# Performance work log

Measured on AMD Instinct MI355X. Metric: run time of the kernel, lower is better.

## Reference

```python
import jax, jax.numpy as jnp
import numpy as np

B, L, D, DK, T = 8192, 64, 512, 64, 128
WIDE_IN = 2 * T + T * T  # 16640


def setup_inputs() -> dict:
    key = jax.random.key(0)
    ks = jax.random.split(key, 24)
    s = 0.02
    inp = {
        "mashup_tags": jax.random.uniform(ks[0], (B, T), jnp.float32),
        "target_api_tags": jax.random.uniform(ks[1], (B, T), jnp.float32),
        "cross_product_tag": jax.random.uniform(ks[2], (B, T * T), jnp.float32),
        "encoded_api_context": jax.random.normal(ks[3], (B, L, D), jnp.float32),
        "candidate_api_description_feature": jax.random.normal(ks[4], (B, D), jnp.float32),
        "mashup_description_feature": jax.random.normal(ks[5], (B, D), jnp.float32),
        "context_len": jax.random.randint(ks[6], (B,), 0, L + 1, jnp.int64 if jax.config.jax_enable_x64 else jnp.int32),
        # attention projections (torch Linear weight layout: [out, in], no bias)
        "W_K": s * jax.random.normal(ks[7], (DK, D), jnp.float32),
        "W_Q": s * jax.random.normal(ks[8], (DK, D), jnp.float32),
        # wide head
        "wide_w": s * jax.random.normal(ks[9], (1, WIDE_IN), jnp.float32),
        "wide_b": jnp.zeros((1,), jnp.float32),
        # deep MLP 1536->512->256->128->1
        "d1_w": s * jax.random.normal(ks[10], (512, 3 * D), jnp.float32),
        "d1_b": jnp.zeros((512,), jnp.float32),
        "d2_w": s * jax.random.normal(ks[11], (256, 512), jnp.float32),
        "d2_b": jnp.zeros((256,), jnp.float32),
        "d3_w": s * jax.random.normal(ks[12], (128, 256), jnp.float32),
        "d3_b": jnp.zeros((128,), jnp.float32),
        "d4_w": s * jax.random.normal(ks[13], (1, 128), jnp.float32),
        "d4_b": jnp.zeros((1,), jnp.float32),
        "wide_weight": jnp.ones((1,), jnp.float32),
        "deep_weight": jnp.ones((1,), jnp.float32),
        "bias": jnp.zeros((1,), jnp.float32),
    }
    return inp


def reference(mashup_tags, target_api_tags, cross_product_tag,
              encoded_api_context, candidate_api_description_feature,
              mashup_description_feature, context_len,
              W_K, W_Q, wide_w, wide_b,
              d1_w, d1_b, d2_w, d2_b, d3_w, d3_b, d4_w, d4_b,
              wide_weight, deep_weight, bias):
    # ---- wide branch ----
    wide_in = jnp.concatenate([mashup_tags, target_api_tags, cross_product_tag], axis=1)
    wide_out = jax.nn.sigmoid(wide_in @ wide_w.T + wide_b)  # (B,1)

    # ---- ragged attention (vectorized masked softmax replaces the Python batch loop) ----
    K = jnp.einsum("bld,kd->blk", encoded_api_context, W_K)          # (B,L,dk)
    Q = candidate_api_description_feature @ W_Q.T                     # (B,dk)
    scores = jnp.einsum("blk,bk->bl", K, Q)                           # (B,L)
    mask = jnp.arange(scores.shape[1])[None, :] < context_len[:, None]
    m = jnp.max(jnp.where(mask, scores, -1e30), axis=-1, keepdims=True)
    e = jnp.where(mask, jnp.exp(scores - m), 0.0)
    denom = jnp.sum(e, axis=-1, keepdims=True)
    probs = e / jnp.maximum(denom, 1e-30)  # rows with length==0 -> all zeros (matches torch zeros fallback)
    api_context = jnp.einsum("bl,bld->bd", probs, encoded_api_context)  # (B,512)

    # ---- deep branch ----
    deep_in = jnp.concatenate([mashup_description_feature, api_context,
                               candidate_api_description_feature], axis=1)  # (B,1536)
    h = jax.nn.relu(deep_in @ d1_w.T + d1_b)
    h = jax.nn.relu(h @ d2_w.T + d2_b)
    h = jax.nn.relu(h @ d3_w.T + d3_b)
    deep_out = h @ d4_w.T + d4_b  # (B,1)

    out = wide_weight * wide_out + deep_weight * deep_out + bias
    return jax.nn.sigmoid(out)
```

## Files before the change

kernel.cpp:

```cpp
#include <hip/hip_runtime.h>

#define Bsz 8192
#define Lctx 64
#define Ddim 512
#define DK 64
#define Ttag 128
#define RQT 2

using f32x4 = __attribute__((ext_vector_type(4))) float;
using bf16x8 = __attribute__((ext_vector_type(8))) short;

__device__ __forceinline__ float wave_sum(float v) {
#pragma unroll
    for (int m = 32; m > 0; m >>= 1) v += __shfl_xor(v, m, 64);
    return v;
}

__device__ __forceinline__ float dot4(float4 a, float4 b) {
    return a.x * b.x + a.y * b.y + a.z * b.z + a.w * b.w;
}

__device__ __forceinline__ unsigned f2bf(float f) {
    unsigned int u = __float_as_uint(f);
    u = u + 0x7fffu + ((u >> 16) & 1u);
    return u >> 16;
}
__device__ __forceinline__ unsigned pack2(float a, float b) {
    return f2bf(a) | (f2bf(b) << 16);
}
__device__ __forceinline__ float bflo(unsigned int v) { return __uint_as_float(v << 16); }
__device__ __forceinline__ float bfhi(unsigned int v) { return __uint_as_float(v & 0xffff0000u); }
__device__ __forceinline__ float bf2f(unsigned short u) { return __uint_as_float((unsigned)u << 16); }

__global__ __launch_bounds__(256) void k_f2bf(
    const float* __restrict__ s, unsigned short* __restrict__ d, int n4)
{
    const int i = blockIdx.x * 256 + threadIdx.x;
    if (i < n4) {
        const float4 v = ((const float4*)s)[i];
        uint2 w;
        w.x = pack2(v.x, v.y);
        w.y = pack2(v.z, v.w);
        *(uint2*)&d[(size_t)i * 4] = w;
    }
}

__global__ __launch_bounds__(256) void k_qtilde(
    const float* __restrict__ C, const float* __restrict__ WQ,
    const float* __restrict__ WK, float* __restrict__ qt)
{
    const int lane = threadIdx.x & 63;
    const int gw = blockIdx.x * 4 + (threadIdx.x >> 6);
    const int b0 = gw * RQT;

    float4 c0[RQT], c1[RQT];
#pragma unroll
    for (int r = 0; r < RQT; ++r) {
        const float4* row = (const float4*)(C + (size_t)(b0 + r) * Ddim);
        c0[r] = row[lane];
        c1[r] = row[64 + lane];
    }
    float tv[RQT];
#pragma unroll
    for (int r = 0; r < RQT; ++r) tv[r] = 0.f;
    for (int k = 0; k < DK; ++k) {
        const float4* wrow = (const float4*)(WQ + (size_t)k * Ddim);
        const float4 w0 = wrow[lane];
        const float4 w1 = wrow[64 + lane];
#pragma unroll
        for (int r = 0; r < RQT; ++r) {
            float p = dot4(c0[r], w0) + dot4(c1[r], w1);
            p = wave_sum(p);
            if (lane == k) tv[r] = p;
        }
    }
    float4 a0[RQT], a1[RQT];
#pragma unroll
    for (int r = 0; r < RQT; ++r) {
        a0[r] = make_float4(0.f, 0.f, 0.f, 0.f);
        a1[r] = make_float4(0.f, 0.f, 0.f, 0.f);
    }
    for (int k = 0; k < DK; ++k) {
        const float4* wrow = (const float4*)(WK + (size_t)k * Ddim);
        const float4 w0 = wrow[lane];
        const float4 w1 = wrow[64 + lane];
#pragma unroll
        for (int r = 0; r < RQT; ++r) {
            const float tk = __shfl(tv[r], k, 64);
            a0[r].x += tk * w0.x; a0[r].y += tk * w0.y;
            a0[r].z += tk * w0.z; a0[r].w += tk * w0.w;
            a1[r].x += tk * w1.x; a1[r].y += tk * w1.y;
            a1[r].z += tk * w1.z; a1[r].w += tk * w1.w;
        }
    }
#pragma unroll
    for (int r = 0; r < RQT; ++r) {
        float4* orow = (float4*)(qt + (size_t)(b0 + r) * Ddim);
        orow[lane] = a0[r];
        orow[64 + lane] = a1[r];
    }
}

__global__ __launch_bounds__(256, 2) void k_attn(
    const float* __restrict__ X, const float* __restrict__ qt,
    const int* __restrict__ clen, const float* __restrict__ mdesc,
    const float* __restrict__ cand, unsigned short* __restrict__ din)
{
    __shared__ float sl[Lctx];
    __shared__ float pl[Lctx];
    __shared__ float part[4][Ddim];

    const int b = blockIdx.x;
    const int tid = threadIdx.x;
    const int wave = tid >> 6, lane = tid & 63;

    const float4* qrow = (const float4*)(qt + (size_t)b * Ddim);
    const float4 q0 = qrow[lane];
    const float4 q1 = qrow[64 + lane];
    const float4* xb = (const float4*)(X + (size_t)b * Lctx * Ddim);

    uint2 pk[16][2];
    float sc[16];

#pragma unroll
    for (int g = 0; g < 4; ++g) {
        float4 t0[4], t1[4];
#pragma unroll
        for (int i = 0; i < 4; ++i) {
            const int l = wave * 16 + g * 4 + i;
            t0[i] = xb[l * 128 + lane];
            t1[i] = xb[l * 128 + 64 + lane];
        }
#pragma unroll
        for (int i = 0; i < 4; ++i) {
            const int r = g * 4 + i;
            sc[r] = dot4(t0[i], q0) + dot4(t1[i], q1);
            pk[r][0].x = pack2(t0[i].x, t0[i].y);
            pk[r][0].y = pack2(t0[i].z, t0[i].w);
            pk[r][1].x = pack2(t1[i].x, t1[i].y);
            pk[r][1].y = pack2(t1[i].z, t1[i].w);
        }
    }
#pragma unroll
    for (int r = 0; r < 16; ++r) sc[r] = wave_sum(sc[r]);
    if (lane == 0) {
#pragma unroll
        for (int r = 0; r < 16; ++r) sl[wave * 16 + r] = sc[r];
    }
    __syncthreads();

    const int len = clen[b];
    float m = -1e30f;
    for (int l = 0; l < len; ++l) m = fmaxf(m, sl[l]);
    float denom = 0.f;
    for (int l = 0; l < len; ++l) denom += __expf(sl[l] - m);
    const float rden = 1.f / fmaxf(denom, 1e-30f);
    if (tid < Lctx) pl[tid] = (tid < len) ? __expf(sl[tid] - m) * rden : 0.f;
    __syncthreads();

    float4 a0 = make_float4(0.f, 0.f, 0.f, 0.f);
    float4 a1 = make_float4(0.f, 0.f, 0.f, 0.f);
#pragma unroll
    for (int r = 0; r < 16; ++r) {
        const float p = pl[wave * 16 + r];
        a0.x += p * bflo(pk[r][0].x); a0.y += p * bfhi(pk[r][0].x);
        a0.z += p * bflo(pk[r][0].y); a0.w += p * bfhi(pk[r][0].y);
        a1.x += p * bflo(pk[r][1].x); a1.y += p * bfhi(pk[r][1].x);
        a1.z += p * bflo(pk[r][1].y); a1.w += p * bfhi(pk[r][1].y);
    }
    *(float4*)&part[wave][lane * 4] = a0;
    *(float4*)&part[wave][256 + lane * 4] = a1;
    __syncthreads();

    unsigned short* dr = din + (size_t)b * 1536;
    {
        const int d0 = tid * 2;
        const float2 s0 = *(const float2*)&part[0][d0];
        const float2 s1 = *(const float2*)&part[1][d0];
        const float2 s2 = *(const float2*)&part[2][d0];
        const float2 s3 = *(const float2*)&part[3][d0];
        const float vx = s0.x + s1.x + s2.x + s3.x;
        const float vy = s0.y + s1.y + s2.y + s3.y;
        *(unsigned*)&dr[512 + d0] = pack2(vx, vy);
    }
    {
        const float4 v = (tid < 128)
            ? ((const float4*)(mdesc + (size_t)b * Ddim))[tid]
            : ((const float4*)(cand + (size_t)b * Ddim))[tid - 128];
        uint2 w;
        w.x = pack2(v.x, v.y);
        w.y = pack2(v.z, v.w);
        const int off = (tid < 128) ? tid * 4 : 1024 + (tid - 128) * 4;
        *(uint2*)&dr[off] = w;
    }
}

__global__ __launch_bounds__(256) void k_wide(
    const float* __restrict__ mt, const float* __restrict__ tt,
    const float* __restrict__ cp, const float* __restrict__ ww,
    const float* __restrict__ wb, float* __restrict__ wl)
{
    const int b = blockIdx.x;
    const int tid = threadIdx.x;
    const int wave = tid >> 6, lane = tid & 63;
    float acc = 0.f;
    if (tid < 64) {
        float4 v;
        if (tid < 32) v = ((const float4*)(mt + (size_t)b * Ttag))[tid];
        else          v = ((const float4*)(tt + (size_t)b * Ttag))[tid - 32];
        const float4 w = ((const float4*)ww)[tid];
        acc += dot4(v, w);
    }
    const float4* cp4 = (const float4*)(cp + (size_t)b * (Ttag * Ttag));
    const float4* ww4 = (const float4*)(ww + 2 * Ttag);
#pragma unroll 4
    for (int i = tid; i < (Ttag * Ttag) / 4; i += 256)
        acc += dot4(cp4[i], ww4[i]);
    acc = wave_sum(acc);
    __shared__ float red[4];
    if (lane == 0) red[wave] = acc;
    __syncthreads();
    if (tid == 0) wl[b] = red[0] + red[1] + red[2] + red[3] + wb[0];
}

__global__ __launch_bounds__(256) void k_gemm_bf16(
    const unsigned short* __restrict__ A, const unsigned short* __restrict__ W,
    const float* __restrict__ bias, unsigned short* __restrict__ C,
    const int K, const int N, const int relu)
{
    __shared__ unsigned short As[128][72];
    __shared__ unsigned short Bs[128][72];
    const int tid = threadIdx.x;
    const int wave = tid >> 6, lane = tid & 63;
    const int wm = wave >> 1, wn = wave & 1;
    const size_t m0 = (size_t)blockIdx.x * 128;
    const size_t n0 = (size_t)blockIdx.y * 128;

    f32x4 acc[4][4];
#pragma unroll
    for (int i = 0; i < 4; ++i)
#pragma unroll
        for (int j = 0; j < 4; ++j) acc[i][j] = (f32x4){0.f, 0.f, 0.f, 0.f};

    uint4 pa[4], pb[4];
    auto loadA = [&](int k0) {
#pragma unroll
        for (int j = 0; j < 4; ++j) {
            const int i = tid + j * 256;
            const int row = i >> 3, c8 = (i & 7) * 8;
            pa[j] = *(const uint4*)(A + (m0 + row) * (size_t)K + k0 + c8);
        }
    };
    auto loadB = [&](int k0) {
#pragma unroll
        for (int j = 0; j < 4; ++j) {
            const int i = tid + j * 256;
            const int row = i >> 3, c8 = (i & 7) * 8;
            pb[j] = *(const uint4*)(W + (n0 + row) * (size_t)K + k0 + c8);
        }
    };

    loadA(0);
    loadB(0);
    for (int k0 = 0; k0 < K; k0 += 64) {
        __syncthreads();
#pragma unroll
        for (int j = 0; j < 4; ++j) {
            const int i = tid + j * 256;
            const int row = i >> 3, c8 = (i & 7) * 8;
            *(uint4*)&As[row][c8] = pa[j];
            *(uint4*)&Bs[row][c8] = pb[j];
        }
        __syncthreads();
        if (k0 + 64 < K) { loadA(k0 + 64); loadB(k0 + 64); }
#pragma unroll
        for (int kk = 0; kk < 2; ++kk) {
            const int krow = kk * 32 + (lane >> 4) * 8;
            bf16x8 af[4], bfr[4];
#pragma unroll
            for (int mm = 0; mm < 4; ++mm)
                af[mm] = *(const bf16x8*)&As[wm * 64 + mm * 16 + (lane & 15)][krow];
#pragma unroll
            for (int nn = 0; nn < 4; ++nn)
                bfr[nn] = *(const bf16x8*)&Bs[wn * 64 + nn * 16 + (lane & 15)][krow];
#pragma unroll
            for (int mm = 0; mm < 4; ++mm)
#pragma unroll
                for (int nn = 0; nn < 4; ++nn)
                    acc[mm][nn] = __builtin_amdgcn_mfma_f32_16x16x32_bf16(
                        af[mm], bfr[nn], acc[mm][nn], 0, 0, 0);
        }
    }

#pragma unroll
    for (int nn = 0; nn < 4; ++nn) {
        const int col = (int)n0 + wn * 64 + nn * 16 + (lane & 15);
        const float bv = bias[col];
#pragma unroll
        for (int mm = 0; mm < 4; ++mm) {
#pragma unroll
            for (int r = 0; r < 4; ++r) {
                const size_t row = m0 + wm * 64 + mm * 16 + (lane >> 4) * 4 + r;
                float v = acc[mm][nn][r] + bv;
                if (relu) v = fmaxf(v, 0.f);
                C[row * N + col] = (unsigned short)f2bf(v);
            }
        }
    }
}

__global__ __launch_bounds__(256) void k_final(
    const unsigned short* __restrict__ h3, const float* __restrict__ d4w,
    const float* __restrict__ d4b, const float* __restrict__ wl,
    const float* __restrict__ wwt, const float* __restrict__ dwt,
    const float* __restrict__ bs, float* __restrict__ out)
{
    const int lane = threadIdx.x & 63;
    const int b = blockIdx.x * 4 + (threadIdx.x >> 6);
    const unsigned short* hr = h3 + (size_t)b * 128;
    float v = bf2f(hr[lane]) * d4w[lane] + bf2f(hr[64 + lane]) * d4w[64 + lane];
    v = wave_sum(v);
    if (lane == 0) {
        const float deep = v + d4b[0];
        const float wo = 1.f / (1.f + __expf(-wl[b]));
        const float z = wwt[0] * wo + dwt[0] * deep + bs[0];
        out[b] = 1.f / (1.f + __expf(-z));
    }
}

extern "C" void kernel_launch(void* const* d_in, const int* in_sizes, int n_in,
                              void* d_out, int out_size, void* d_ws, size_t ws_size,
                              hipStream_t stream)
{
    const float* mt    = (const float*)d_in[0];
    const float* tt    = (const float*)d_in[1];
    const float* cp    = (const float*)d_in[2];
    const float* X     = (const float*)d_in[3];
    const float* cand  = (const float*)d_in[4];
    const float* mdesc = (const float*)d_in[5];
    const int*   clen  = (const int*)d_in[6];
    const float* WK    = (const float*)d_in[7];
    const float* WQ    = (const float*)d_in[8];
    const float* ww    = (const float*)d_in[9];
    const float* wb    = (const float*)d_in[10];
    const float* d1w   = (const float*)d_in[11];
    const float* d1b   = (const float*)d_in[12];
    const float* d2w   = (const float*)d_in[13];
    const float* d2b   = (const float*)d_in[14];
    const float* d3w   = (const float*)d_in[15];
    const float* d3b   = (const float*)d_in[16];
    const float* d4w   = (const float*)d_in[17];
    const float* d4b   = (const float*)d_in[18];
    const float* wwt   = (const float*)d_in[19];
    const float* dwt   = (const float*)d_in[20];
    const float* bs    = (const float*)d_in[21];
    float* out = (float*)d_out;

    char* w = (char*)d_ws;
    unsigned short* din = (unsigned short*)w;            w += (size_t)Bsz * 1536 * 2;
    float* qt           = (float*)w;                     w += (size_t)Bsz * 512 * 4;
    unsigned short* h1  = (unsigned short*)w;            w += (size_t)Bsz * 512 * 2;
    unsigned short* h2  = (unsigned short*)w;            w += (size_t)Bsz * 256 * 2;
    unsigned short* h3  = (unsigned short*)w;            w += (size_t)Bsz * 128 * 2;
    float* wl           = (float*)w;                     w += (size_t)Bsz * 4;
    unsigned short* w1b = (unsigned short*)w;            w += (size_t)512 * 1536 * 2;
    unsigned short* w2b = (unsigned short*)w;            w += (size_t)256 * 512 * 2;
    unsigned short* w3b = (unsigned short*)w;            w += (size_t)128 * 256 * 2;

    hipLaunchKernelGGL(k_f2bf, dim3(768), dim3(256), 0, stream, d1w, w1b, 512 * 1536 / 4);
    hipLaunchKernelGGL(k_f2bf, dim3(128), dim3(256), 0, stream, d2w, w2b, 256 * 512 / 4);
    hipLaunchKernelGGL(k_f2bf, dim3(32),  dim3(256), 0, stream, d3w, w3b, 128 * 256 / 4);

    hipLaunchKernelGGL(k_qtilde, dim3(Bsz / (RQT * 4)), dim3(256), 0, stream,
                       cand, WQ, WK, qt);
    hipLaunchKernelGGL(k_attn, dim3(Bsz), dim3(256), 0, stream,
                       X, qt, clen, mdesc, cand, din);
    hipLaunchKernelGGL(k_wide, dim3(Bsz), dim3(256), 0, stream,
                       mt, tt, cp, ww, wb, wl);
    hipLaunchKernelGGL(k_gemm_bf16, dim3(64, 4), dim3(256), 0, stream,
                       din, w1b, d1b, h1, 1536, 512, 1);
    hipLaunchKernelGGL(k_gemm_bf16, dim3(64, 2), dim3(256), 0, stream,
                       h1, w2b, d2b, h2, 512, 256, 1);
    hipLaunchKernelGGL(k_gemm_bf16, dim3(64, 1), dim3(256), 0, stream,
                       h2, w3b, d3b, h3, 256, 128, 1);
    hipLaunchKernelGGL(k_final, dim3(Bsz / 4), dim3(256), 0, stream,
                       h3, d4w, d4b, wl, wwt, dwt, bs, out);
}
```

Before: 473.9 us.

## Skip masked context rows, fuse wide head into attention, merge weight casts

The attention kernel now loads, scores and accumulates only context rows below context_len, so masked rows of the large encoded context tensor are never read from memory. The wide-branch dot product over the cross-product tags is folded into the same per-row kernel, removing one launch and overlapping its loads with the attention work. The three weight-cast kernels are merged into one launch. The risks are extra register pressure in the fused kernel and divergent predicated loads.

```diff
diff --git a/kernel.cpp b/kernel.cpp
--- a/kernel.cpp
+++ b/kernel.cpp
@@ -32,17 +32,23 @@
 __device__ __forceinline__ float bfhi(unsigned int v) { return __uint_as_float(v & 0xffff0000u); }
 __device__ __forceinline__ float bf2f(unsigned short u) { return __uint_as_float((unsigned)u << 16); }
 
-__global__ __launch_bounds__(256) void k_f2bf(
-    const float* __restrict__ s, unsigned short* __restrict__ d, int n4)
-{
-    const int i = blockIdx.x * 256 + threadIdx.x;
-    if (i < n4) {
-        const float4 v = ((const float4*)s)[i];
-        uint2 w;
-        w.x = pack2(v.x, v.y);
-        w.y = pack2(v.z, v.w);
-        *(uint2*)&d[(size_t)i * 4] = w;
-    }
+__global__ __launch_bounds__(256) void k_f2bf3(
+    const float* __restrict__ s1, unsigned short* __restrict__ d1,
+    const float* __restrict__ s2, unsigned short* __restrict__ d2,
+    const float* __restrict__ s3, unsigned short* __restrict__ d3)
+{
+    int i = blockIdx.x * 256 + threadIdx.x;
+    const float* s;
+    unsigned short* d;
+    if (i < 196608)      { s = s1; d = d1; }
+    else if (i < 229376) { i -= 196608; s = s2; d = d2; }
+    else if (i < 237568) { i -= 229376; s = s3; d = d3; }
+    else return;
+    const float4 v = ((const float4*)s)[i];
+    uint2 w;
+    w.x = pack2(v.x, v.y);
+    w.y = pack2(v.z, v.w);
+    *(uint2*)&d[(size_t)i * 4] = w;
 }
 
 __global__ __launch_bounds__(256) void k_qtilde(
@@ -101,18 +107,25 @@
     }
 }
 
-__global__ __launch_bounds__(256, 2) void k_attn(
+__global__ __launch_bounds__(256, 2) void k_attn_wide(
     const float* __restrict__ X, const float* __restrict__ qt,
     const int* __restrict__ clen, const float* __restrict__ mdesc,
-    const float* __restrict__ cand, unsigned short* __restrict__ din)
+    const float* __restrict__ cand,
+    const float* __restrict__ mt, const float* __restrict__ tt,
+    const float* __restrict__ cp, const float* __restrict__ ww,
+    const float* __restrict__ wb,
+    unsigned short* __restrict__ din, float* __restrict__ wl)
 {
     __shared__ float sl[Lctx];
     __shared__ float pl[Lctx];
     __shared__ float part[4][Ddim];
+    __shared__ float red[4];
 
     const int b = blockIdx.x;
     const int tid = threadIdx.x;
     const int wave = tid >> 6, lane = tid & 63;
+    const int len = clen[b];
+    const int nrows = min(16, max(0, len - wave * 16));
 
     const float4* qrow = (const float4*)(qt + (size_t)b * Ddim);
     const float4 q0 = qrow[lane];
@@ -124,32 +137,57 @@
 
 #pragma unroll
     for (int g = 0; g < 4; ++g) {
-        float4 t0[4], t1[4];
-#pragma unroll
-        for (int i = 0; i < 4; ++i) {
-            const int l = wave * 16 + g * 4 + i;
-            t0[i] = xb[l * 128 + lane];
-            t1[i] = xb[l * 128 + 64 + lane];
-        }
-#pragma unroll
-        for (int i = 0; i < 4; ++i) {
-            const int r = g * 4 + i;
-            sc[r] = dot4(t0[i], q0) + dot4(t1[i], q1);
-            pk[r][0].x = pack2(t0[i].x, t0[i].y);
-            pk[r][0].y = pack2(t0[i].z, t0[i].w);
-            pk[r][1].x = pack2(t1[i].x, t1[i].y);
-            pk[r][1].y = pack2(t1[i].z, t1[i].w);
-        }
-    }
-#pragma unroll
-    for (int r = 0; r < 16; ++r) sc[r] = wave_sum(sc[r]);
+        if (g * 4 < nrows) {
+            float4 t0[4], t1[4];
+#pragma unroll
+            for (int i = 0; i < 4; ++i) {
+                if (g * 4 + i < nrows) {
+                    const int l = wave * 16 + g * 4 + i;
+                    t0[i] = xb[l * 128 + lane];
+                    t1[i] = xb[l * 128 + 64 + lane];
+                }
+            }
+#pragma unroll
+            for (int i = 0; i < 4; ++i) {
+                if (g * 4 + i < nrows) {
+                    const int r = g * 4 + i;
+                    sc[r] = dot4(t0[i], q0) + dot4(t1[i], q1);
+                    pk[r][0].x = pack2(t0[i].x, t0[i].y);
+                    pk[r][0].y = pack2(t0[i].z, t0[i].w);
+                    pk[r][1].x = pack2(t1[i].x, t1[i].y);
+                    pk[r][1].y = pack2(t1[i].z, t1[i].w);
+                }
+            }
+        }
+    }
+#pragma unroll
+    for (int r = 0; r < 16; ++r)
+        if (r < nrows) sc[r] = wave_sum(sc[r]);
     if (lane == 0) {
 #pragma unroll
-        for (int r = 0; r < 16; ++r) sl[wave * 16 + r] = sc[r];
-    }
+        for (int r = 0; r < 16; ++r)
+            if (r < nrows) sl[wave * 16 + r] = sc[r];
+    }
+
+    float wacc = 0.f;
+    if (tid < 64) {
+        float4 v;
+        if (tid < 32) v = ((const float4*)(mt + (size_t)b * Ttag))[tid];
+        else          v = ((const float4*)(tt + (size_t)b * Ttag))[tid - 32];
+        wacc += dot4(v, ((const float4*)ww)[tid]);
+    }
+    {
+        const float4* cp4 = (const float4*)(cp + (size_t)b * (Ttag * Ttag));
+        const float4* ww4 = (const float4*)(ww + 2 * Ttag);
+#pragma unroll 4
+        for (int i = tid; i < (Ttag * Ttag) / 4; i += 256)
+            wacc += dot4(cp4[i], ww4[i]);
+    }
+    wacc = wave_sum(wacc);
+    if (lane == 0) red[wave] = wacc;
+
     __syncthreads();
 
-    const int len = clen[b];
     float m = -1e30f;
     for (int l = 0; l < len; ++l) m = fmaxf(m, sl[l]);
     float denom = 0.f;
@@ -162,11 +200,13 @@
     float4 a1 = make_float4(0.f, 0.f, 0.f, 0.f);
 #pragma unroll
     for (int r = 0; r < 16; ++r) {
-        const float p = pl[wave * 16 + r];
-        a0.x += p * bflo(pk[r][0].x); a0.y += p * bfhi(pk[r][0].x);
-        a0.z += p * bflo(pk[r][0].y); a0.w += p * bfhi(pk[r][0].y);
-        a1.x += p * bflo(pk[r][1].x); a1.y += p * bfhi(pk[r][1].x);
-        a1.z += p * bflo(pk[r][1].y); a1.w += p * bfhi(pk[r][1].y);
+        if (r < nrows) {
+            const float p = pl[wave * 16 + r];
+            a0.x += p * bflo(pk[r][0].x); a0.y += p * bfhi(pk[r][0].x);
+            a0.z += p * bflo(pk[r][0].y); a0.w += p * bfhi(pk[r][0].y);
+            a1.x += p * bflo(pk[r][1].x); a1.y += p * bfhi(pk[r][1].x);
+            a1.z += p * bflo(pk[r][1].y); a1.w += p * bfhi(pk[r][1].y);
+        }
     }
     *(float4*)&part[wave][lane * 4] = a0;
     *(float4*)&part[wave][256 + lane * 4] = a1;
@@ -193,33 +233,6 @@
         const int off = (tid < 128) ? tid * 4 : 1024 + (tid - 128) * 4;
         *(uint2*)&dr[off] = w;
     }
-}
-
-__global__ __launch_bounds__(256) void k_wide(
-    const float* __restrict__ mt, const float* __restrict__ tt,
-    const float* __restrict__ cp, const float* __restrict__ ww,
-    const float* __restrict__ wb, float* __restrict__ wl)
-{
-    const int b = blockIdx.x;
-    const int tid = threadIdx.x;
-    const int wave = tid >> 6, lane = tid & 63;
-    float acc = 0.f;
-    if (tid < 64) {
-        float4 v;
-        if (tid < 32) v = ((const float4*)(mt + (size_t)b * Ttag))[tid];
-        else          v = ((const float4*)(tt + (size_t)b * Ttag))[tid - 32];
-        const float4 w = ((const float4*)ww)[tid];
-        acc += dot4(v, w);
-    }
-    const float4* cp4 = (const float4*)(cp + (size_t)b * (Ttag * Ttag));
-    const float4* ww4 = (const float4*)(ww + 2 * Ttag);
-#pragma unroll 4
-    for (int i = tid; i < (Ttag * Ttag) / 4; i += 256)
-        acc += dot4(cp4[i], ww4[i]);
-    acc = wave_sum(acc);
-    __shared__ float red[4];
-    if (lane == 0) red[wave] = acc;
-    __syncthreads();
     if (tid == 0) wl[b] = red[0] + red[1] + red[2] + red[3] + wb[0];
 }
 
@@ -367,16 +380,12 @@
     unsigned short* w2b = (unsigned short*)w;            w += (size_t)256 * 512 * 2;
     unsigned short* w3b = (unsigned short*)w;            w += (size_t)128 * 256 * 2;
 
-    hipLaunchKernelGGL(k_f2bf, dim3(768), dim3(256), 0, stream, d1w, w1b, 512 * 1536 / 4);
-    hipLaunchKernelGGL(k_f2bf, dim3(128), dim3(256), 0, stream, d2w, w2b, 256 * 512 / 4);
-    hipLaunchKernelGGL(k_f2bf, dim3(32),  dim3(256), 0, stream, d3w, w3b, 128 * 256 / 4);
-
+    hipLaunchKernelGGL(k_f2bf3, dim3(928), dim3(256), 0, stream,
+                       d1w, w1b, d2w, w2b, d3w, w3b);
     hipLaunchKernelGGL(k_qtilde, dim3(Bsz / (RQT * 4)), dim3(256), 0, stream,
                        cand, WQ, WK, qt);
-    hipLaunchKernelGGL(k_attn, dim3(Bsz), dim3(256), 0, stream,
-                       X, qt, clen, mdesc, cand, din);
-    hipLaunchKernelGGL(k_wide, dim3(Bsz), dim3(256), 0, stream,
-                       mt, tt, cp, ww, wb, wl);
+    hipLaunchKernelGGL(k_attn_wide, dim3(Bsz), dim3(256), 0, stream,
+                       X, qt, clen, mdesc, cand, mt, tt, cp, ww, wb, din, wl);
     hipLaunchKernelGGL(k_gemm_bf16, dim3(64, 4), dim3(256), 0, stream,
                        din, w1b, d1b, h1, 1536, 512, 1);
     hipLaunchKernelGGL(k_gemm_bf16, dim3(64, 2), dim3(256), 0, stream,
```

Result: faster. 443.2 us (-6.5%).
